# Performance work log

Hardware: AMD Instinct MI355X
Metric: run time of the kernel (lower is better)

## Reference

```python
import jax, jax.numpy as jnp
import numpy as np

N_HEADS = 16
LN_EPS = 1e-6


def _mha(q_in, kv_in, mask, wq, bq, wk, bk, wv, bv, wo, bo):
    B, Sq, D = q_in.shape
    H = N_HEADS
    dh = D // H
    def split(x):  # [B,S,D] -> [B,H,S,dh]
        return x.reshape(B, -1, H, dh).transpose(0, 2, 1, 3)
    q = split(q_in @ wq + bq)
    k = split(kv_in @ wk + bk)
    v = split(kv_in @ wv + bv)
    scores = jnp.einsum('bhqd,bhkd->bhqk', q, k) / jnp.sqrt(jnp.asarray(dh, q.dtype))
    scores = scores + mask * (-1e9)
    attn = jax.nn.softmax(scores, axis=-1)
    out = jnp.einsum('bhqk,bhkd->bhqd', attn, v)
    out = out.transpose(0, 2, 1, 3).reshape(B, Sq, D)
    return out @ wo + bo


def _layer_norm(x, gamma, beta):
    mu = jnp.mean(x, axis=-1, keepdims=True)
    var = jnp.mean(jnp.square(x - mu), axis=-1, keepdims=True)
    return (x - mu) * jax.lax.rsqrt(var + LN_EPS) * gamma + beta


def setup_inputs() -> dict:
    key = jax.random.key(0)
    B, S_dec, S_enc, D, F = 4, 1024, 1024, 1024, 4096
    ks = jax.random.split(key, 16)
    s = 0.02
    inp = {
        'inputs': jax.random.normal(ks[0], (B, S_dec, D), jnp.float32),
        'enc_outputs': jax.random.normal(ks[1], (B, S_enc, D), jnp.float32),
        # causal look-ahead mask: 1 above diagonal -> -1e9 added to scores
        'mask_1': jnp.triu(jnp.ones((S_dec, S_dec), jnp.float32), k=1)[None, None],
        'mask_2': jnp.zeros((B, 1, 1, S_enc), jnp.float32),
    }
    names = ['wq1', 'wk1', 'wv1', 'wo1', 'wq2', 'wk2', 'wv2', 'wo2']
    for i, n in enumerate(names):
        inp[n] = jax.random.normal(ks[2 + i], (D, D), jnp.float32) * s
        inp['b' + n[1:]] = jnp.zeros((D,), jnp.float32)
    inp['w_ff1'] = jax.random.normal(ks[10], (D, F), jnp.float32) * s
    inp['b_ff1'] = jnp.zeros((F,), jnp.float32)
    inp['w_ff2'] = jax.random.normal(ks[11], (F, D), jnp.float32) * s
    inp['b_ff2'] = jnp.zeros((D,), jnp.float32)
    for i in (1, 2, 3):
        inp[f'g{i}'] = jnp.ones((D,), jnp.float32)
        inp[f'beta{i}'] = jnp.zeros((D,), jnp.float32)
    return inp


def reference(inputs, enc_outputs, mask_1, mask_2,
              wq1, bq1, wk1, bk1, wv1, bv1, wo1, bo1,
              wq2, bq2, wk2, bk2, wv2, bv2, wo2, bo2,
              w_ff1, b_ff1, w_ff2, b_ff2,
              g1, beta1, g2, beta2, g3, beta3):
    # causal self-attention + residual + LN (dropout inactive at inference)
    attn = _mha(inputs, inputs, mask_1, wq1, bq1, wk1, bk1, wv1, bv1, wo1, bo1)
    attn = _layer_norm(attn + inputs, g1, beta1)
    # encoder-decoder cross-attention + residual + LN
    attn2 = _mha(attn, enc_outputs, mask_2, wq2, bq2, wk2, bk2, wv2, bv2, wo2, bo2)
    attn2 = _layer_norm(attn2 + attn, g2, beta2)
    # FFN + residual + LN
    h = jax.nn.relu(attn2 @ w_ff1 + b_ff1)
    h = h @ w_ff2 + b_ff2
    return _layer_norm(h + attn2, g3, beta3)
```

## Files before the change

kernel.cpp:

```cpp
#include <hip/hip_runtime.h>
#include <stdint.h>

typedef unsigned short ushort_t;
typedef __attribute__((ext_vector_type(8))) short bf16x8;
typedef __attribute__((ext_vector_type(4))) float f32x4;
typedef __attribute__((ext_vector_type(4))) unsigned short us4;

#define DEV __device__ __forceinline__

DEV unsigned short f2bf(float f) {
  union { float f; unsigned u; } x; x.f = f;
  unsigned r = x.u + 0x7fffu + ((x.u >> 16) & 1u);
  return (unsigned short)(r >> 16);
}

DEV void gload16(const void* g, void* l) {
  __builtin_amdgcn_global_load_lds(
      (const __attribute__((address_space(1))) unsigned int*)g,
      (__attribute__((address_space(3))) unsigned int*)l, 16, 0, 0);
}

__global__ __launch_bounds__(256) void cast_bf16_kernel(
    const float* __restrict__ x, ushort_t* __restrict__ y, int n4) {
  int i = blockIdx.x * 256 + threadIdx.x;
  if (i >= n4) return;
  float4 v = ((const float4*)x)[i];
  us4 o; o.x = f2bf(v.x); o.y = f2bf(v.y); o.z = f2bf(v.z); o.w = f2bf(v.w);
  ((us4*)y)[i] = o;
}

__global__ __launch_bounds__(256) void reduce_cast_kernel(
    const float* __restrict__ p0, const float* __restrict__ p1,
    ushort_t* __restrict__ y, int n4) {
  int i = blockIdx.x * 256 + threadIdx.x;
  if (i >= n4) return;
  float4 a = ((const float4*)p0)[i];
  float4 b = ((const float4*)p1)[i];
  us4 o; o.x = f2bf(a.x + b.x); o.y = f2bf(a.y + b.y);
  o.z = f2bf(a.z + b.z); o.w = f2bf(a.w + b.w);
  ((us4*)y)[i] = o;
}

__global__ __launch_bounds__(256) void transpose_cast_kernel(
    const float* __restrict__ W, ushort_t* __restrict__ dst, int K, int N) {
  __shared__ float tile[64][65];
  int n0 = blockIdx.x * 64, k0 = blockIdx.y * 64;
  int tid = threadIdx.x;
#pragma unroll
  for (int it = 0; it < 16; ++it) {
    int idx = it * 256 + tid; int r = idx >> 6, c = idx & 63;
    tile[r][c] = W[(size_t)(k0 + r) * N + n0 + c];
  }
  __syncthreads();
#pragma unroll
  for (int it = 0; it < 16; ++it) {
    int idx = it * 256 + tid; int r = idx >> 6, c = idx & 63;
    dst[(size_t)(n0 + r) * K + k0 + c] = f2bf(tile[c][r]);
  }
}

struct Src8 { const float* p[8]; };
__global__ __launch_bounds__(256) void transpose_cast8_kernel(
    Src8 s, ushort_t* __restrict__ dst) {
  __shared__ float tile[64][65];
  const float* W = s.p[blockIdx.z];
  ushort_t* out = dst + (size_t)blockIdx.z * 1048576;
  int n0 = blockIdx.x * 64, k0 = blockIdx.y * 64;
  int tid = threadIdx.x;
#pragma unroll
  for (int it = 0; it < 16; ++it) {
    int idx = it * 256 + tid; int r = idx >> 6, c = idx & 63;
    tile[r][c] = W[(size_t)(k0 + r) * 1024 + n0 + c];
  }
  __syncthreads();
#pragma unroll
  for (int it = 0; it < 16; ++it) {
    int idx = it * 256 + tid; int r = idx >> 6, c = idx & 63;
    out[(size_t)(n0 + r) * 1024 + k0 + c] = f2bf(tile[c][r]);
  }
}

__global__ __launch_bounds__(256) void transpose_v_kernel(
    const ushort_t* __restrict__ V, int ldv, ushort_t* __restrict__ vT) {
  __shared__ ushort_t tile[64][65];
  int s0 = blockIdx.x * 64;
  int bh = blockIdx.y;
  int b = bh >> 4, h = bh & 15;
  int tid = threadIdx.x;
#pragma unroll
  for (int it = 0; it < 4; ++it) {
    int idx = it * 256 + tid; int r = idx >> 4, c = (idx & 15) * 4;
    us4 v = *(const us4*)&V[(size_t)(b * 1024 + s0 + r) * ldv + h * 64 + c];
    tile[r][c] = v.x; tile[r][c + 1] = v.y; tile[r][c + 2] = v.z; tile[r][c + 3] = v.w;
  }
  __syncthreads();
#pragma unroll
  for (int it = 0; it < 4; ++it) {
    int idx = it * 256 + tid; int r = idx >> 4, c = (idx & 15) * 4;
    us4 o; o.x = tile[c][r]; o.y = tile[c + 1][r]; o.z = tile[c + 2][r]; o.w = tile[c + 3][r];
    *(us4*)&vT[((size_t)bh * 64 + r) * 1024 + s0 + c] = o;
  }
}

template <int WF32, int WB16, int RELU>
__global__ __launch_bounds__(256, 2) void gemm_bt(
    const ushort_t* __restrict__ A, const ushort_t* __restrict__ Bt,
    const float* __restrict__ b0, const float* __restrict__ b1,
    const float* __restrict__ b2, const float* __restrict__ b3,
    float* __restrict__ Cf, ushort_t* __restrict__ Cb,
    int M, int N, int K, int Ks, long long pstr) {
  __shared__ ushort_t sA[4096];
  __shared__ ushort_t sB[4096];
  const int tid = threadIdx.x;
  const int w = tid >> 6, lane = tid & 63;
  const int lrow = lane & 15, lk = lane >> 4;
  const int m0 = blockIdx.x * 128, n0 = blockIdx.y * 128;
  const int kz = blockIdx.z * Ks;
  const int wr = w >> 1, wc = w & 1;
  f32x4 acc[4][4] = {};
  const int brow0 = (w * 1024 + lane * 16) >> 6;
  const int kbyte = (lane * 16) & 63;

  for (int kt = kz; kt < kz + Ks; kt += 32) {
    __syncthreads();
    const ushort_t* ga = A + (size_t)(m0 + brow0) * K + kt + (kbyte >> 1);
    gload16(ga, (char*)sA + w * 1024);
    gload16(ga + (size_t)64 * K, (char*)sA + 4096 + w * 1024);
    const ushort_t* gb = Bt + (size_t)(n0 + brow0) * K + kt + (kbyte >> 1);
    gload16(gb, (char*)sB + w * 1024);
    gload16(gb + (size_t)64 * K, (char*)sB + 4096 + w * 1024);
    __syncthreads();
    bf16x8 aF[4], bF[4];
#pragma unroll
    for (int t = 0; t < 4; ++t) {
      aF[t] = *(const bf16x8*)((const char*)sA + ((wr * 64 + t * 16 + lrow) << 6) + (lk << 4));
      bF[t] = *(const bf16x8*)((const char*)sB + ((wc * 64 + t * 16 + lrow) << 6) + (lk << 4));
    }
#pragma unroll
    for (int mt = 0; mt < 4; ++mt)
#pragma unroll
      for (int nt = 0; nt < 4; ++nt)
        acc[mt][nt] = __builtin_amdgcn_mfma_f32_16x16x32_bf16(aF[mt], bF[nt], acc[mt][nt], 0, 0, 0);
  }
  float* Cfz = Cf + (long long)blockIdx.z * pstr;
#pragma unroll
  for (int nt = 0; nt < 4; ++nt) {
    int col = n0 + wc * 64 + nt * 16 + lrow;
    int seg = col >> 10;
    const float* bp = seg == 0 ? b0 : seg == 1 ? b1 : seg == 2 ? b2 : b3;
    float bv = bp[col & 1023];
    if (blockIdx.z != 0) bv = 0.f;
#pragma unroll
    for (int mt = 0; mt < 4; ++mt) {
      int rowb = m0 + wr * 64 + mt * 16 + lk * 4;
#pragma unroll
      for (int j = 0; j < 4; ++j) {
        float v = acc[mt][nt][j] + bv;
        if (RELU) v = fmaxf(v, 0.f);
        size_t idx = (size_t)(rowb + j) * N + col;
        if (WF32) Cfz[idx] = v;
        if (WB16) Cb[idx] = f2bf(v);
      }
    }
  }
}

template <int CAUSAL>
__global__ __launch_bounds__(256, 4) void attn_kernel(
    const ushort_t* __restrict__ Q, int ldq,
    const ushort_t* __restrict__ Kp, int ldk,
    const ushort_t* __restrict__ vT,
    const float* __restrict__ mask2,
    ushort_t* __restrict__ O) {
  __shared__ ushort_t sK[2][4096];
  __shared__ ushort_t sV[2][4096];
  __shared__ ushort_t sP[4][1024];
  const int qb = blockIdx.x, bh = blockIdx.y;
  const int b = bh >> 4, h = bh & 15;
  const int tid = threadIdx.x, w = tid >> 6, lane = tid & 63;
  const int lrow = lane & 15, lk = lane >> 4;

  const ushort_t* qptr = Q + (size_t)(b * 1024 + qb * 64 + w * 16 + lrow) * ldq + h * 64 + lk * 8;
  bf16x8 qF0 = *(const bf16x8*)qptr;
  bf16x8 qF1 = *(const bf16x8*)(qptr + 32);
  f32x4 oacc[4] = {};
  float m_[4], l_[4];
#pragma unroll
  for (int j = 0; j < 4; ++j) { m_[j] = -3.0e38f; l_[j] = 0.f; }
  const int nkb = CAUSAL ? (qb + 1) : 16;
  const float C = 0.18033688011112042f;

  const int sr = w * 16 + (lane >> 3);
  const int scb = (((lane & 7) ^ (lane >> 3)) * 16);
  const ushort_t* kbase = Kp + (size_t)(b * 1024 + sr) * ldk + h * 64 + (scb >> 1);
  const ushort_t* vbase = vT + ((size_t)bh * 64 + sr) * 1024 + (scb >> 1);
  char* dstK0 = (char*)sK[0] + w * 2048;
  char* dstV0 = (char*)sV[0] + w * 2048;

#define STAGE(kb_, bufi)                                              \
  do {                                                                \
    const ushort_t* gk = kbase + (size_t)(kb_) * 64 * ldk;            \
    gload16(gk, dstK0 + (bufi) * 8192);                               \
    gload16(gk + (size_t)8 * ldk, dstK0 + (bufi) * 8192 + 1024);      \
    const ushort_t* gv = vbase + (kb_) * 64;                          \
    gload16(gv, dstV0 + (bufi) * 8192);                               \
    gload16(gv + (size_t)8 * 1024, dstV0 + (bufi) * 8192 + 1024);     \
  } while (0)

  STAGE(0, 0);
  const int swz = (lrow & 7) << 4;

  for (int kb = 0; kb < nkb; ++kb) {
    const int buf = kb & 1;
    __syncthreads();
    if (kb + 1 < nkb) STAGE(kb + 1, buf ^ 1);

    const char* kB = (const char*)sK[buf];
    const char* vB = (const char*)sV[buf];
    f32x4 sc[4];
#pragma unroll
    for (int kt = 0; kt < 4; ++kt) {
      const char* rp = kB + ((kt * 16 + lrow) << 7);
      bf16x8 k0 = *(const bf16x8*)(rp + ((lk * 16) ^ swz));
      bf16x8 k1 = *(const bf16x8*)(rp + ((64 + lk * 16) ^ swz));
      f32x4 z = {};
      z = __builtin_amdgcn_mfma_f32_16x16x32_bf16(qF0, k0, z, 0, 0, 0);
      sc[kt] = __builtin_amdgcn_mfma_f32_16x16x32_bf16(qF1, k1, z, 0, 0, 0);
    }
    float mv[4];
    if (!CAUSAL) {
#pragma unroll
      for (int kt = 0; kt < 4; ++kt)
        mv[kt] = mask2[b * 1024 + kb * 64 + kt * 16 + lrow];
    }
#pragma unroll
    for (int j = 0; j < 4; ++j) {
      float s0 = sc[0][j], s1 = sc[1][j], s2 = sc[2][j], s3 = sc[3][j];
      if (CAUSAL) {
        if (kb == qb) {
          int qr = w * 16 + lk * 4 + j;
          if (lrow > qr) s0 = -3.0e38f;
          if (16 + lrow > qr) s1 = -3.0e38f;
          if (32 + lrow > qr) s2 = -3.0e38f;
          if (48 + lrow > qr) s3 = -3.0e38f;
        }
      } else {
        s0 = fmaf(mv[0], -8e9f, s0);
        s1 = fmaf(mv[1], -8e9f, s1);
        s2 = fmaf(mv[2], -8e9f, s2);
        s3 = fmaf(mv[3], -8e9f, s3);
      }
      float mx = fmaxf(fmaxf(s0, s1), fmaxf(s2, s3));
      mx = fmaxf(mx, __shfl_xor(mx, 1));
      mx = fmaxf(mx, __shfl_xor(mx, 2));
      mx = fmaxf(mx, __shfl_xor(mx, 4));
      mx = fmaxf(mx, __shfl_xor(mx, 8));
      float mnew = fmaxf(m_[j], mx);
      float scale = __builtin_exp2f((m_[j] - mnew) * C);
      float e0 = __builtin_exp2f((s0 - mnew) * C);
      float e1 = __builtin_exp2f((s1 - mnew) * C);
      float e2 = __builtin_exp2f((s2 - mnew) * C);
      float e3 = __builtin_exp2f((s3 - mnew) * C);
      float ps = (e0 + e1) + (e2 + e3);
      ps += __shfl_xor(ps, 1);
      ps += __shfl_xor(ps, 2);
      ps += __shfl_xor(ps, 4);
      ps += __shfl_xor(ps, 8);
      l_[j] = l_[j] * scale + ps;
      m_[j] = mnew;
      oacc[0][j] *= scale; oacc[1][j] *= scale;
      oacc[2][j] *= scale; oacc[3][j] *= scale;
      int qp = lk * 4 + j;
      char* bp = (char*)sP[w] + qp * 128;
      int sz = (qp & 7) << 4;
      *(ushort_t*)(bp + ((lrow * 2) ^ sz)) = f2bf(e0);
      *(ushort_t*)(bp + ((32 + lrow * 2) ^ sz)) = f2bf(e1);
      *(ushort_t*)(bp + ((64 + lrow * 2) ^ sz)) = f2bf(e2);
      *(ushort_t*)(bp + ((96 + lrow * 2) ^ sz)) = f2bf(e3);
    }
    const char* pB = (const char*)sP[w] + (lrow << 7);
    bf16x8 pF0 = *(const bf16x8*)(pB + ((lk * 16) ^ swz));
    bf16x8 pF1 = *(const bf16x8*)(pB + ((64 + lk * 16) ^ swz));
#pragma unroll
    for (int t = 0; t < 4; ++t) {
      const char* rp = vB + ((t * 16 + lrow) << 7);
      bf16x8 v0 = *(const bf16x8*)(rp + ((lk * 16) ^ swz));
      bf16x8 v1 = *(const bf16x8*)(rp + ((64 + lk * 16) ^ swz));
      oacc[t] = __builtin_amdgcn_mfma_f32_16x16x32_bf16(pF0, v0, oacc[t], 0, 0, 0);
      oacc[t] = __builtin_amdgcn_mfma_f32_16x16x32_bf16(pF1, v1, oacc[t], 0, 0, 0);
    }
  }
#undef STAGE
#pragma unroll
  for (int j = 0; j < 4; ++j) {
    float invl = 1.f / l_[j];
    int row = qb * 64 + w * 16 + lk * 4 + j;
    ushort_t* op = O + (size_t)(b * 1024 + row) * 1024 + h * 64;
#pragma unroll
    for (int t = 0; t < 4; ++t) op[t * 16 + lrow] = f2bf(oacc[t][j] * invl);
  }
}

template <int WB16, int NPART>
__global__ __launch_bounds__(256) void ln_kernel(
    const float* __restrict__ p0, const float* __restrict__ p1,
    const float* __restrict__ p2, const float* __restrict__ p3,
    const float* __restrict__ r,
    const float* __restrict__ g, const float* __restrict__ be,
    float* __restrict__ yf, ushort_t* __restrict__ yb) {
  int row = blockIdx.x, tid = threadIdx.x;
  size_t off = (size_t)row * 1024;
  float4 va = ((const float4*)(p0 + off))[tid];
  if (NPART >= 2) {
    float4 t = ((const float4*)(p1 + off))[tid];
    va.x += t.x; va.y += t.y; va.z += t.z; va.w += t.w;
  }
  if (NPART >= 4) {
    float4 t2 = ((const float4*)(p2 + off))[tid];
    float4 t3 = ((const float4*)(p3 + off))[tid];
    va.x += t2.x + t3.x; va.y += t2.y + t3.y;
    va.z += t2.z + t3.z; va.w += t2.w + t3.w;
  }
  float4 vb = ((const float4*)(r + off))[tid];
  float x0 = va.x + vb.x, x1 = va.y + vb.y, x2 = va.z + vb.z, x3 = va.w + vb.w;
  float s = x0 + x1 + x2 + x3;
  float s2 = x0 * x0 + x1 * x1 + x2 * x2 + x3 * x3;
#pragma unroll
  for (int o = 1; o < 64; o <<= 1) { s += __shfl_xor(s, o); s2 += __shfl_xor(s2, o); }
  __shared__ float sh[8];
  if ((tid & 63) == 0) { sh[tid >> 6] = s; sh[4 + (tid >> 6)] = s2; }
  __syncthreads();
  s = sh[0] + sh[1] + sh[2] + sh[3];
  s2 = sh[4] + sh[5] + sh[6] + sh[7];
  float mu = s * 0.0009765625f;
  float var = s2 * 0.0009765625f - mu * mu;
  float inv = rsqrtf(var + 1e-6f);
  float4 gv = ((const float4*)g)[tid];
  float4 bv = ((const float4*)be)[tid];
  float y0 = (x0 - mu) * inv * gv.x + bv.x;
  float y1 = (x1 - mu) * inv * gv.y + bv.y;
  float y2 = (x2 - mu) * inv * gv.z + bv.z;
  float y3 = (x3 - mu) * inv * gv.w + bv.w;
  ((float4*)(yf + off))[tid] = make_float4(y0, y1, y2, y3);
  if (WB16) {
    us4 o; o.x = f2bf(y0); o.y = f2bf(y1); o.z = f2bf(y2); o.w = f2bf(y3);
    ((us4*)(yb + off))[tid] = o;
  }
}

extern "C" void kernel_launch(void* const* d_in, const int* in_sizes, int n_in,
                              void* d_out, int out_size, void* d_ws, size_t ws_size,
                              hipStream_t stream) {
  (void)in_sizes; (void)n_in; (void)out_size; (void)ws_size;
  const float* inputs = (const float*)d_in[0];
  const float* enc    = (const float*)d_in[1];
  const float* mask2  = (const float*)d_in[3];
  const float* wq1 = (const float*)d_in[4];  const float* bq1 = (const float*)d_in[5];
  const float* wk1 = (const float*)d_in[6];  const float* bk1 = (const float*)d_in[7];
  const float* wv1 = (const float*)d_in[8];  const float* bv1 = (const float*)d_in[9];
  const float* wo1 = (const float*)d_in[10]; const float* bo1 = (const float*)d_in[11];
  const float* wq2 = (const float*)d_in[12]; const float* bq2 = (const float*)d_in[13];
  const float* wk2 = (const float*)d_in[14]; const float* bk2 = (const float*)d_in[15];
  const float* wv2 = (const float*)d_in[16]; const float* bv2 = (const float*)d_in[17];
  const float* wo2 = (const float*)d_in[18]; const float* bo2 = (const float*)d_in[19];
  const float* wff1 = (const float*)d_in[20]; const float* bff1 = (const float*)d_in[21];
  const float* wff2 = (const float*)d_in[22]; const float* bff2 = (const float*)d_in[23];
  const float* g1 = (const float*)d_in[24]; const float* be1 = (const float*)d_in[25];
  const float* g2 = (const float*)d_in[26]; const float* be2 = (const float*)d_in[27];
  const float* g3 = (const float*)d_in[28]; const float* be3 = (const float*)d_in[29];

  char* ws = (char*)d_ws;
  const size_t MB = 1024 * 1024;
  const size_t W1M = 1048576;
  ushort_t* wt    = (ushort_t*)ws;
  ushort_t* xb    = (ushort_t*)(ws + 32 * MB);
  ushort_t* encb  = (ushort_t*)(ws + 40 * MB);
  ushort_t* qkvb  = (ushort_t*)(ws + 48 * MB);
  ushort_t* vtb   = (ushort_t*)(ws + 72 * MB);
  ushort_t* attnb = (ushort_t*)(ws + 80 * MB);
  ushort_t* y1b   = (ushort_t*)(ws + 88 * MB);
  ushort_t* y2b   = (ushort_t*)(ws + 96 * MB);
  float*    c1f   = (float*)(ws + 104 * MB);
  float*    p48f  = (float*)(ws + 48 * MB);
  float*    y1f   = (float*)(ws + 120 * MB);
  float*    y2f   = (float*)(ws + 136 * MB);
  ushort_t* q2b   = (ushort_t*)(ws + 32 * MB);
  ushort_t* kv2b  = (ushort_t*)(ws + 56 * MB);
  ushort_t* hb    = (ushort_t*)(ws + 32 * MB);
  float*    pff   = (float*)(ws + 72 * MB);
  float* outf = (float*)d_out;
  const long long PELEMS = 4 * 1024 * 1024;
  const long long P48OFF = (long long)(p48f - c1f);

  cast_bf16_kernel<<<4096, 256, 0, stream>>>(inputs, xb, 1048576);
  cast_bf16_kernel<<<4096, 256, 0, stream>>>(enc, encb, 1048576);
  Src8 s8; s8.p[0] = wq1; s8.p[1] = wk1; s8.p[2] = wv1; s8.p[3] = wo1;
           s8.p[4] = wq2; s8.p[5] = wk2; s8.p[6] = wv2; s8.p[7] = wo2;
  transpose_cast8_kernel<<<dim3(16, 16, 8), 256, 0, stream>>>(s8, wt);
  transpose_cast_kernel<<<dim3(64, 16), 256, 0, stream>>>(wff1, wt + 8 * W1M, 1024, 4096);
  transpose_cast_kernel<<<dim3(16, 64), 256, 0, stream>>>(wff2, wt + 12 * W1M, 4096, 1024);

  gemm_bt<0, 1, 0><<<dim3(32, 24, 1), 256, 0, stream>>>(
      xb, wt, bq1, bk1, bv1, bv1, nullptr, qkvb, 4096, 3072, 1024, 1024, 0);
  transpose_v_kernel<<<dim3(16, 64), 256, 0, stream>>>(qkvb + 2048, 3072, vtb);
  attn_kernel<1><<<dim3(16, 64), 256, 0, stream>>>(
      qkvb, 3072, qkvb + 1024, 3072, vtb, nullptr, attnb);
  gemm_bt<1, 0, 0><<<dim3(32, 8, 2), 256, 0, stream>>>(
      attnb, wt + 3 * W1M, bo1, bo1, bo1, bo1, c1f, nullptr, 4096, 1024, 1024, 512, P48OFF);
  ln_kernel<1, 2><<<4096, 256, 0, stream>>>(c1f, p48f, nullptr, nullptr,
                                            inputs, g1, be1, y1f, y1b);

  gemm_bt<1, 0, 0><<<dim3(32, 8, 2), 256, 0, stream>>>(
      y1b, wt + 4 * W1M, bq2, bq2, bq2, bq2, c1f, nullptr, 4096, 1024, 1024, 512, P48OFF);
  reduce_cast_kernel<<<4096, 256, 0, stream>>>(c1f, p48f, q2b, 1048576);
  gemm_bt<0, 1, 0><<<dim3(32, 16, 1), 256, 0, stream>>>(
      encb, wt + 5 * W1M, bk2, bv2, bk2, bk2, nullptr, kv2b, 4096, 2048, 1024, 1024, 0);
  transpose_v_kernel<<<dim3(16, 64), 256, 0, stream>>>(kv2b + 1024, 2048, vtb);
  attn_kernel<0><<<dim3(16, 64), 256, 0, stream>>>(
      q2b, 1024, kv2b, 2048, vtb, mask2, attnb);
  gemm_bt<1, 0, 0><<<dim3(32, 8, 2), 256, 0, stream>>>(
      attnb, wt + 7 * W1M, bo2, bo2, bo2, bo2, c1f, nullptr, 4096, 1024, 1024, 512, P48OFF);
  ln_kernel<1, 2><<<4096, 256, 0, stream>>>(c1f, p48f, nullptr, nullptr,
                                            y1f, g2, be2, y2f, y2b);

  gemm_bt<0, 1, 1><<<dim3(32, 32, 1), 256, 0, stream>>>(
      y2b, wt + 8 * W1M, bff1, bff1 + 1024, bff1 + 2048, bff1 + 3072,
      nullptr, hb, 4096, 4096, 1024, 1024, 0);
  gemm_bt<1, 0, 0><<<dim3(32, 8, 4), 256, 0, stream>>>(
      hb, wt + 12 * W1M, bff2, bff2, bff2, bff2, pff, nullptr,
      4096, 1024, 4096, 1024, PELEMS);
  ln_kernel<0, 4><<<4096, 256, 0, stream>>>(pff, pff + PELEMS, pff + 2 * PELEMS,
                                            pff + 3 * PELEMS, y2f, g3, be3, outf, nullptr);
}
```

Baseline: 424.4 us.

## Transpose attention score MFMA so softmax reductions stay in-lane, skip rescale

Measured after the change: 373.1 us. -12.1%, faster.

```diff
diff --git a/kernel.cpp b/kernel.cpp
--- a/kernel.cpp
+++ b/kernel.cpp
@@ -175,7 +175,7 @@
   __shared__ ushort_t sK[2][4096];
   __shared__ ushort_t sV[2][4096];
   __shared__ ushort_t sP[4][1024];
-  const int qb = blockIdx.x, bh = blockIdx.y;
+  const int bh = blockIdx.x, qb = blockIdx.y;
   const int b = bh >> 4, h = bh & 15;
   const int tid = threadIdx.x, w = tid >> 6, lane = tid & 63;
   const int lrow = lane & 15, lk = lane >> 4;
@@ -184,9 +184,7 @@
   bf16x8 qF0 = *(const bf16x8*)qptr;
   bf16x8 qF1 = *(const bf16x8*)(qptr + 32);
   f32x4 oacc[4] = {};
-  float m_[4], l_[4];
-#pragma unroll
-  for (int j = 0; j < 4; ++j) { m_[j] = -3.0e38f; l_[j] = 0.f; }
+  float m_ = -3.0e38f, l_ = 0.f;
   const int nkb = CAUSAL ? (qb + 1) : 16;
   const float C = 0.18033688011112042f;
 
@@ -218,69 +216,76 @@
     const char* kB = (const char*)sK[buf];
     const char* vB = (const char*)sV[buf];
     f32x4 sc[4];
+    __builtin_amdgcn_s_setprio(1);
 #pragma unroll
     for (int kt = 0; kt < 4; ++kt) {
       const char* rp = kB + ((kt * 16 + lrow) << 7);
       bf16x8 k0 = *(const bf16x8*)(rp + ((lk * 16) ^ swz));
       bf16x8 k1 = *(const bf16x8*)(rp + ((64 + lk * 16) ^ swz));
       f32x4 z = {};
-      z = __builtin_amdgcn_mfma_f32_16x16x32_bf16(qF0, k0, z, 0, 0, 0);
-      sc[kt] = __builtin_amdgcn_mfma_f32_16x16x32_bf16(qF1, k1, z, 0, 0, 0);
-    }
-    float mv[4];
-    if (!CAUSAL) {
-#pragma unroll
-      for (int kt = 0; kt < 4; ++kt)
-        mv[kt] = mask2[b * 1024 + kb * 64 + kt * 16 + lrow];
-    }
-#pragma unroll
-    for (int j = 0; j < 4; ++j) {
-      float s0 = sc[0][j], s1 = sc[1][j], s2 = sc[2][j], s3 = sc[3][j];
-      if (CAUSAL) {
-        if (kb == qb) {
-          int qr = w * 16 + lk * 4 + j;
-          if (lrow > qr) s0 = -3.0e38f;
-          if (16 + lrow > qr) s1 = -3.0e38f;
-          if (32 + lrow > qr) s2 = -3.0e38f;
-          if (48 + lrow > qr) s3 = -3.0e38f;
-        }
-      } else {
-        s0 = fmaf(mv[0], -8e9f, s0);
-        s1 = fmaf(mv[1], -8e9f, s1);
-        s2 = fmaf(mv[2], -8e9f, s2);
-        s3 = fmaf(mv[3], -8e9f, s3);
+      z = __builtin_amdgcn_mfma_f32_16x16x32_bf16(k0, qF0, z, 0, 0, 0);
+      sc[kt] = __builtin_amdgcn_mfma_f32_16x16x32_bf16(k1, qF1, sc[kt] = z, 0, 0, 0);
+    }
+    __builtin_amdgcn_s_setprio(0);
+    if (CAUSAL) {
+      if (kb == qb) {
+        int ql = w * 16 + lrow;
+#pragma unroll
+        for (int kt = 0; kt < 4; ++kt)
+#pragma unroll
+          for (int j = 0; j < 4; ++j)
+            if (kt * 16 + lk * 4 + j > ql) sc[kt][j] = -3.0e38f;
       }
-      float mx = fmaxf(fmaxf(s0, s1), fmaxf(s2, s3));
-      mx = fmaxf(mx, __shfl_xor(mx, 1));
-      mx = fmaxf(mx, __shfl_xor(mx, 2));
-      mx = fmaxf(mx, __shfl_xor(mx, 4));
-      mx = fmaxf(mx, __shfl_xor(mx, 8));
-      float mnew = fmaxf(m_[j], mx);
-      float scale = __builtin_exp2f((m_[j] - mnew) * C);
-      float e0 = __builtin_exp2f((s0 - mnew) * C);
-      float e1 = __builtin_exp2f((s1 - mnew) * C);
-      float e2 = __builtin_exp2f((s2 - mnew) * C);
-      float e3 = __builtin_exp2f((s3 - mnew) * C);
-      float ps = (e0 + e1) + (e2 + e3);
-      ps += __shfl_xor(ps, 1);
-      ps += __shfl_xor(ps, 2);
-      ps += __shfl_xor(ps, 4);
-      ps += __shfl_xor(ps, 8);
-      l_[j] = l_[j] * scale + ps;
-      m_[j] = mnew;
-      oacc[0][j] *= scale; oacc[1][j] *= scale;
-      oacc[2][j] *= scale; oacc[3][j] *= scale;
-      int qp = lk * 4 + j;
-      char* bp = (char*)sP[w] + qp * 128;
-      int sz = (qp & 7) << 4;
-      *(ushort_t*)(bp + ((lrow * 2) ^ sz)) = f2bf(e0);
-      *(ushort_t*)(bp + ((32 + lrow * 2) ^ sz)) = f2bf(e1);
-      *(ushort_t*)(bp + ((64 + lrow * 2) ^ sz)) = f2bf(e2);
-      *(ushort_t*)(bp + ((96 + lrow * 2) ^ sz)) = f2bf(e3);
-    }
-    const char* pB = (const char*)sP[w] + (lrow << 7);
-    bf16x8 pF0 = *(const bf16x8*)(pB + ((lk * 16) ^ swz));
-    bf16x8 pF1 = *(const bf16x8*)(pB + ((64 + lk * 16) ^ swz));
+    } else {
+#pragma unroll
+      for (int kt = 0; kt < 4; ++kt) {
+        float4 mv = *(const float4*)&mask2[b * 1024 + kb * 64 + kt * 16 + lk * 4];
+        sc[kt][0] = fmaf(mv.x, -8e9f, sc[kt][0]);
+        sc[kt][1] = fmaf(mv.y, -8e9f, sc[kt][1]);
+        sc[kt][2] = fmaf(mv.z, -8e9f, sc[kt][2]);
+        sc[kt][3] = fmaf(mv.w, -8e9f, sc[kt][3]);
+      }
+    }
+    float mx = fmaxf(fmaxf(fmaxf(sc[0][0], sc[0][1]), fmaxf(sc[0][2], sc[0][3])),
+                     fmaxf(fmaxf(sc[1][0], sc[1][1]), fmaxf(sc[1][2], sc[1][3])));
+    mx = fmaxf(mx, fmaxf(fmaxf(fmaxf(sc[2][0], sc[2][1]), fmaxf(sc[2][2], sc[2][3])),
+                         fmaxf(fmaxf(sc[3][0], sc[3][1]), fmaxf(sc[3][2], sc[3][3]))));
+    mx = fmaxf(mx, __shfl_xor(mx, 16));
+    mx = fmaxf(mx, __shfl_xor(mx, 32));
+    float mnew = fmaxf(m_, mx);
+    float scale = __builtin_exp2f((m_ - mnew) * C);
+    float ps = 0.f;
+#pragma unroll
+    for (int kt = 0; kt < 4; ++kt)
+#pragma unroll
+      for (int j = 0; j < 4; ++j) {
+        float e = __builtin_exp2f((sc[kt][j] - mnew) * C);
+        sc[kt][j] = e;
+        ps += e;
+      }
+    ps += __shfl_xor(ps, 16);
+    ps += __shfl_xor(ps, 32);
+    l_ = l_ * scale + ps;
+    m_ = mnew;
+    if (__any(scale < 1.f)) {
+#pragma unroll
+      for (int j = 0; j < 4; ++j) {
+        float sj = __shfl(scale, lk * 4 + j);
+        oacc[0][j] *= sj; oacc[1][j] *= sj; oacc[2][j] *= sj; oacc[3][j] *= sj;
+      }
+    }
+    char* bp = (char*)sP[w] + lrow * 128;
+#pragma unroll
+    for (int kt = 0; kt < 4; ++kt) {
+      unsigned d0, d1;
+      asm("v_cvt_pk_bf16_f32 %0, %1, %2" : "=v"(d0) : "v"(sc[kt][0]), "v"(sc[kt][1]));
+      asm("v_cvt_pk_bf16_f32 %0, %1, %2" : "=v"(d1) : "v"(sc[kt][2]), "v"(sc[kt][3]));
+      uint2 dd; dd.x = d0; dd.y = d1;
+      *(uint2*)(bp + ((kt * 32 + lk * 8) ^ swz)) = dd;
+    }
+    bf16x8 pF0 = *(const bf16x8*)(bp + ((lk * 16) ^ swz));
+    bf16x8 pF1 = *(const bf16x8*)(bp + ((64 + lk * 16) ^ swz));
+    __builtin_amdgcn_s_setprio(1);
 #pragma unroll
     for (int t = 0; t < 4; ++t) {
       const char* rp = vB + ((t * 16 + lrow) << 7);
@@ -289,11 +294,13 @@
       oacc[t] = __builtin_amdgcn_mfma_f32_16x16x32_bf16(pF0, v0, oacc[t], 0, 0, 0);
       oacc[t] = __builtin_amdgcn_mfma_f32_16x16x32_bf16(pF1, v1, oacc[t], 0, 0, 0);
     }
+    __builtin_amdgcn_s_setprio(0);
   }
 #undef STAGE
 #pragma unroll
   for (int j = 0; j < 4; ++j) {
-    float invl = 1.f / l_[j];
+    float lj = __shfl(l_, lk * 4 + j);
+    float invl = 1.f / lj;
     int row = qb * 64 + w * 16 + lk * 4 + j;
     ushort_t* op = O + (size_t)(b * 1024 + row) * 1024 + h * 64;
 #pragma unroll
@@ -403,7 +410,7 @@
   gemm_bt<0, 1, 0><<<dim3(32, 24, 1), 256, 0, stream>>>(
       xb, wt, bq1, bk1, bv1, bv1, nullptr, qkvb, 4096, 3072, 1024, 1024, 0);
   transpose_v_kernel<<<dim3(16, 64), 256, 0, stream>>>(qkvb + 2048, 3072, vtb);
-  attn_kernel<1><<<dim3(16, 64), 256, 0, stream>>>(
+  attn_kernel<1><<<dim3(64, 16), 256, 0, stream>>>(
       qkvb, 3072, qkvb + 1024, 3072, vtb, nullptr, attnb);
   gemm_bt<1, 0, 0><<<dim3(32, 8, 2), 256, 0, stream>>>(
       attnb, wt + 3 * W1M, bo1, bo1, bo1, bo1, c1f, nullptr, 4096, 1024, 1024, 512, P48OFF);
@@ -416,7 +423,7 @@
   gemm_bt<0, 1, 0><<<dim3(32, 16, 1), 256, 0, stream>>>(
       encb, wt + 5 * W1M, bk2, bv2, bk2, bk2, nullptr, kv2b, 4096, 2048, 1024, 1024, 0);
   transpose_v_kernel<<<dim3(16, 64), 256, 0, stream>>>(kv2b + 1024, 2048, vtb);
-  attn_kernel<0><<<dim3(16, 64), 256, 0, stream>>>(
+  attn_kernel<0><<<dim3(64, 16), 256, 0, stream>>>(
       q2b, 1024, kv2b, 2048, vtb, mask2, attnb);
   gemm_bt<1, 0, 0><<<dim3(32, 8, 2), 256, 0, stream>>>(
       attnb, wt + 7 * W1M, bo2, bo2, bo2, bo2, c1f, nullptr, 4096, 1024, 1024, 512, P48OFF);
```
